# Optimization experiments

Hardware: AMD Instinct MI355X
Metric: run time of the kernel (lower is better)

Reference implementation:

```python
import jax, jax.numpy as jnp
import numpy as np

N, NTIMES, D_FEAT = 2048, 32, 128


def setup_inputs() -> dict:
    key = jax.random.key(0)
    k1, k2 = jax.random.split(key)
    return {
        "target_fairness": jnp.zeros((), dtype=jnp.float32),
        "prediction": jax.random.uniform(k1, (N, NTIMES), dtype=jnp.float32),
        "X_distance": jax.random.normal(k2, (N, D_FEAT), dtype=jnp.float32),
        "ntimes": NTIMES,
        "scale": jnp.ones((), dtype=jnp.float32),
    }


def reference(target_fairness, prediction, X_distance, ntimes, scale):
    n = prediction.shape[0]
    # cosine distance matrix: 1 - cos_sim, matches sklearn cosine_distances
    norms = jnp.linalg.norm(X_distance, axis=1, keepdims=True)
    Xn = X_distance / norms
    dist = 1.0 - Xn @ Xn.T  # [N, N]
    # pairwise |pred_j - pred_k| over all time points: [N, N, T]
    diff = jnp.abs(prediction[:, None, :] - prediction[None, :, :])
    hinge = jnp.maximum(0.0, diff - scale * dist[:, :, None])
    # only pairs k > j contribute
    mask = jnp.triu(jnp.ones((n, n), dtype=bool), k=1)
    R_beta = jnp.sum(jnp.where(mask[:, :, None], hinge, 0.0))
    model_fairness = 2.0 * R_beta / (n * (n - 1) * ntimes)
    return jnp.maximum(0.0, model_fairness - target_fairness)
```

## Files before the change

kernel.cpp:

```cpp
#include <hip/hip_runtime.h>

#define N 2048
#define T 32
#define D 128
#define BT 32
#define MT (N / BT)
#define NTILES (MT * (MT + 1) / 2)
#define NWAVES (2 * NTILES)
#define PSTR 33

typedef float floatx4 __attribute__((ext_vector_type(4)));
typedef short bf16x8 __attribute__((ext_vector_type(8)));

#define LGKM0() __builtin_amdgcn_s_waitcnt(0xc07f)

__device__ __forceinline__ void split8(float4 a, float4 b, bf16x8& h, bf16x8& l) {
  float v[8] = {a.x, a.y, a.z, a.w, b.x, b.y, b.z, b.w};
#pragma unroll
  for (int i = 0; i < 8; ++i) {
    unsigned u = __float_as_uint(v[i]);
    h[i] = (short)(u >> 16);
    float lo = v[i] - __uint_as_float(u & 0xffff0000u);
    l[i] = (short)(__float_as_uint(lo) >> 16);
  }
}

__device__ __forceinline__ float sumsq8(float4 a, float4 b) {
  return a.x * a.x + a.y * a.y + a.z * a.z + a.w * a.w +
         b.x * b.x + b.y * b.y + b.z * b.z + b.w * b.w;
}

__device__ __forceinline__ void tile_decode(int t, int& a, int& b) {
  a = (int)((2 * MT + 1 -
             sqrtf((float)((2 * MT + 1) * (2 * MT + 1) - 8 * t))) * 0.5f);
  while (a > 0 && t < a * MT - a * (a - 1) / 2) --a;
  while (t >= (a + 1) * MT - (a + 1) * a / 2) ++a;
  b = a + (t - (a * MT - a * (a - 1) / 2));
}

__global__ __launch_bounds__(64) void pair_kernel(
    const float* __restrict__ pred,
    const float* __restrict__ X,
    const float* __restrict__ scale_p,
    double* __restrict__ partials) {
  __shared__ float P[48 * PSTR];
  __shared__ float nrmA[16], nrmB[32];

  const int lane = threadIdx.x;
  const int w    = blockIdx.x;
  const int tile = w >> 1;
  const int h    = w & 1;

  int a, b;
  tile_decode(tile, a, b);
  const int aRow0 = a * BT, bRow0 = b * BT;
  const int m    = lane & 15;
  const int quad = lane >> 4;
  const float scale = scale_p[0];

#pragma unroll
  for (int s = 0; s < 6; ++s) {
    const int idx = s * 64 + lane;
    const int row = idx >> 3;
    const int fo  = (idx & 7) * 4;
    const int grow = (row < 16) ? (aRow0 + 16 * h + row) : (bRow0 + row - 16);
    *(float4*)(&P[row * PSTR + fo]) =
        *(const float4*)(pred + (size_t)grow * T + fo);
  }

  floatx4 accf[2];
  accf[0] = (floatx4){0.f, 0.f, 0.f, 0.f};
  accf[1] = (floatx4){0.f, 0.f, 0.f, 0.f};
  float ssA = 0.f, ssB[2] = {0.f, 0.f};

  const float* xar = X + (size_t)(aRow0 + 16 * h + m) * D + quad * 8;
  const float* xb0 = X + (size_t)(bRow0 + m) * D + quad * 8;

#pragma unroll
  for (int ks = 0; ks < 4; ++ks) {
    bf16x8 hA, lA, hB[2], lB[2];
    {
      float4 u0 = *(const float4*)(xar + ks * 32);
      float4 u1 = *(const float4*)(xar + ks * 32 + 4);
      ssA += sumsq8(u0, u1);
      split8(u0, u1, hA, lA);
    }
#pragma unroll
    for (int J = 0; J < 2; ++J) {
      float4 w0 = *(const float4*)(xb0 + (size_t)J * 16 * D + ks * 32);
      float4 w1 = *(const float4*)(xb0 + (size_t)J * 16 * D + ks * 32 + 4);
      ssB[J] += sumsq8(w0, w1);
      split8(w0, w1, hB[J], lB[J]);
    }
#pragma unroll
    for (int J = 0; J < 2; ++J) {
      accf[J] = __builtin_amdgcn_mfma_f32_16x16x32_bf16(hA, hB[J], accf[J], 0, 0, 0);
      accf[J] = __builtin_amdgcn_mfma_f32_16x16x32_bf16(hA, lB[J], accf[J], 0, 0, 0);
      accf[J] = __builtin_amdgcn_mfma_f32_16x16x32_bf16(lA, hB[J], accf[J], 0, 0, 0);
    }
  }

  ssA += __shfl_xor(ssA, 16, 64);
  ssA += __shfl_xor(ssA, 32, 64);
#pragma unroll
  for (int J = 0; J < 2; ++J) {
    ssB[J] += __shfl_xor(ssB[J], 16, 64);
    ssB[J] += __shfl_xor(ssB[J], 32, 64);
  }
  if (quad == 0) {
    nrmA[m]      = rsqrtf(ssA);
    nrmB[m]      = rsqrtf(ssB[0]);
    nrmB[16 + m] = rsqrtf(ssB[1]);
  }
  LGKM0();

  float na[4], nb[2];
#pragma unroll
  for (int r = 0; r < 4; ++r) na[r] = nrmA[quad * 4 + r];
  nb[0] = nrmB[m];
  nb[1] = nrmB[16 + m];

  float sd[2][4], ps[2][4];
#pragma unroll
  for (int J = 0; J < 2; ++J)
#pragma unroll
    for (int r = 0; r < 4; ++r) {
      sd[J][r] = scale * (1.0f - accf[J][r] * na[r] * nb[J]);
      ps[J][r] = 0.0f;
    }

#pragma unroll
  for (int t4 = 0; t4 < 8; ++t4) {
    float4 qb[2];
    qb[0] = *(const float4*)(&P[(16 + m) * PSTR + t4 * 4]);
    qb[1] = *(const float4*)(&P[(32 + m) * PSTR + t4 * 4]);
#pragma unroll
    for (int r = 0; r < 4; ++r) {
      float4 qa = *(const float4*)(&P[(quad * 4 + r) * PSTR + t4 * 4]);
#pragma unroll
      for (int J = 0; J < 2; ++J) {
        float s = sd[J][r];
        ps[J][r] += fmaxf(fabsf(qa.x - qb[J].x), s) +
                    fmaxf(fabsf(qa.y - qb[J].y), s) +
                    fmaxf(fabsf(qa.z - qb[J].z), s) +
                    fmaxf(fabsf(qa.w - qb[J].w), s);
      }
    }
  }

  float tsum = 0.0f;
#pragma unroll
  for (int J = 0; J < 2; ++J)
#pragma unroll
    for (int r = 0; r < 4; ++r) {
      const int ja   = aRow0 + 16 * h + quad * 4 + r;
      const int kcol = bRow0 + 16 * J + m;
      tsum += (kcol > ja) ? (ps[J][r] - 32.0f * sd[J][r]) : 0.0f;
    }

  double dsum = (double)tsum;
#pragma unroll
  for (int off = 32; off > 0; off >>= 1) dsum += __shfl_down(dsum, off, 64);
  if (lane == 0) partials[w] = dsum;
}

__global__ __launch_bounds__(256) void finalize_kernel(
    const double* __restrict__ partials, const float* __restrict__ target,
    float* __restrict__ out) {
  __shared__ double red[4];
  double s = 0.0;
  for (int i = threadIdx.x; i < NWAVES; i += 256) s += partials[i];
#pragma unroll
  for (int off = 32; off > 0; off >>= 1) s += __shfl_down(s, off, 64);
  int wave = threadIdx.x >> 6, lane = threadIdx.x & 63;
  if (lane == 0) red[wave] = s;
  __syncthreads();
  if (threadIdx.x == 0) {
    double tot = red[0] + red[1] + red[2] + red[3];
    double mf  = 2.0 * tot / ((double)N * (double)(N - 1) * (double)T);
    double r   = mf - (double)target[0];
    out[0] = (float)(r > 0.0 ? r : 0.0);
  }
}

extern "C" void kernel_launch(void* const* d_in, const int* in_sizes, int n_in,
                              void* d_out, int out_size, void* d_ws, size_t ws_size,
                              hipStream_t stream) {
  const float* target = (const float*)d_in[0];
  const float* pred   = (const float*)d_in[1];
  const float* X      = (const float*)d_in[2];
  const float* scale  = (const float*)d_in[4];

  double* partials = (double*)d_ws;

  pair_kernel<<<dim3(NWAVES), dim3(64), 0, stream>>>(pred, X, scale, partials);
  finalize_kernel<<<dim3(1), dim3(256), 0, stream>>>(partials, target,
                                                     (float*)d_out);
}
```

Before: 86.96 us.

## Pre-normalize and pre-split X into bf16 hi/lo in MFMA fragment layout

A new pre-pass kernel normalizes each row of X, splits it into bf16 high and low parts, and writes them in the exact per-lane fragment layout the MFMA loop consumes. The pair kernel then loads ready-made bf16x8 fragments instead of reloading fp32 X, recomputing norms and redoing the split for every tile, and it no longer needs the shared-memory norm exchange. This removes redundant per-tile conversion work and halves the bytes read per fragment. The cost is an extra kernel launch and workspace traffic, and normalizing before the split changes rounding slightly.

```diff
diff --git a/kernel.cpp b/kernel.cpp
--- a/kernel.cpp
+++ b/kernel.cpp
@@ -14,22 +14,6 @@
 
 #define LGKM0() __builtin_amdgcn_s_waitcnt(0xc07f)
 
-__device__ __forceinline__ void split8(float4 a, float4 b, bf16x8& h, bf16x8& l) {
-  float v[8] = {a.x, a.y, a.z, a.w, b.x, b.y, b.z, b.w};
-#pragma unroll
-  for (int i = 0; i < 8; ++i) {
-    unsigned u = __float_as_uint(v[i]);
-    h[i] = (short)(u >> 16);
-    float lo = v[i] - __uint_as_float(u & 0xffff0000u);
-    l[i] = (short)(__float_as_uint(lo) >> 16);
-  }
-}
-
-__device__ __forceinline__ float sumsq8(float4 a, float4 b) {
-  return a.x * a.x + a.y * a.y + a.z * a.z + a.w * a.w +
-         b.x * b.x + b.y * b.y + b.z * b.z + b.w * b.w;
-}
-
 __device__ __forceinline__ void tile_decode(int t, int& a, int& b) {
   a = (int)((2 * MT + 1 -
              sqrtf((float)((2 * MT + 1) * (2 * MT + 1) - 8 * t))) * 0.5f);
@@ -38,13 +22,56 @@
   b = a + (t - (a * MT - a * (a - 1) / 2));
 }
 
+__global__ __launch_bounds__(64) void presplit_kernel(
+    const float* __restrict__ X, unsigned short* __restrict__ hXt,
+    unsigned short* __restrict__ lXt) {
+  const int rb   = blockIdx.x;
+  const int lane = threadIdx.x;
+  const int m    = lane & 15;
+  const int q    = lane >> 4;
+
+  const float* xr = X + (size_t)(16 * rb + m) * D + q * 8;
+  float4 v0[4], v1[4];
+  float ss = 0.0f;
+#pragma unroll
+  for (int ks = 0; ks < 4; ++ks) {
+    v0[ks] = *(const float4*)(xr + ks * 32);
+    v1[ks] = *(const float4*)(xr + ks * 32 + 4);
+    ss += v0[ks].x * v0[ks].x + v0[ks].y * v0[ks].y +
+          v0[ks].z * v0[ks].z + v0[ks].w * v0[ks].w +
+          v1[ks].x * v1[ks].x + v1[ks].y * v1[ks].y +
+          v1[ks].z * v1[ks].z + v1[ks].w * v1[ks].w;
+  }
+  ss += __shfl_xor(ss, 16, 64);
+  ss += __shfl_xor(ss, 32, 64);
+  const float rn = rsqrtf(ss);
+
+#pragma unroll
+  for (int ks = 0; ks < 4; ++ks) {
+    bf16x8 h, l;
+    float v[8] = {v0[ks].x, v0[ks].y, v0[ks].z, v0[ks].w,
+                  v1[ks].x, v1[ks].y, v1[ks].z, v1[ks].w};
+#pragma unroll
+    for (int i = 0; i < 8; ++i) {
+      const float a = v[i] * rn;
+      const unsigned u = __float_as_uint(a);
+      h[i] = (short)(u >> 16);
+      const float lo = a - __uint_as_float(u & 0xffff0000u);
+      l[i] = (short)(__float_as_uint(lo) >> 16);
+    }
+    const size_t o = (size_t)rb * 2048 + ks * 512 + q * 128 + m * 8;
+    *(bf16x8*)(hXt + o) = h;
+    *(bf16x8*)(lXt + o) = l;
+  }
+}
+
 __global__ __launch_bounds__(64) void pair_kernel(
     const float* __restrict__ pred,
-    const float* __restrict__ X,
+    const unsigned short* __restrict__ hXt,
+    const unsigned short* __restrict__ lXt,
     const float* __restrict__ scale_p,
     double* __restrict__ partials) {
   __shared__ float P[48 * PSTR];
-  __shared__ float nrmA[16], nrmB[32];
 
   const int lane = threadIdx.x;
   const int w    = blockIdx.x;
@@ -71,26 +98,24 @@
   floatx4 accf[2];
   accf[0] = (floatx4){0.f, 0.f, 0.f, 0.f};
   accf[1] = (floatx4){0.f, 0.f, 0.f, 0.f};
-  float ssA = 0.f, ssB[2] = {0.f, 0.f};
-
-  const float* xar = X + (size_t)(aRow0 + 16 * h + m) * D + quad * 8;
-  const float* xb0 = X + (size_t)(bRow0 + m) * D + quad * 8;
+
+  const int arb = aRow0 / 16 + h;
+  const int brb = bRow0 / 16;
+  const size_t fo = (size_t)quad * 128 + m * 8;
+  const unsigned short* pa_h = hXt + (size_t)arb * 2048 + fo;
+  const unsigned short* pa_l = lXt + (size_t)arb * 2048 + fo;
+  const unsigned short* pb_h = hXt + (size_t)brb * 2048 + fo;
+  const unsigned short* pb_l = lXt + (size_t)brb * 2048 + fo;
 
 #pragma unroll
   for (int ks = 0; ks < 4; ++ks) {
     bf16x8 hA, lA, hB[2], lB[2];
-    {
-      float4 u0 = *(const float4*)(xar + ks * 32);
-      float4 u1 = *(const float4*)(xar + ks * 32 + 4);
-      ssA += sumsq8(u0, u1);
-      split8(u0, u1, hA, lA);
-    }
+    hA = *(const bf16x8*)(pa_h + ks * 512);
+    lA = *(const bf16x8*)(pa_l + ks * 512);
 #pragma unroll
     for (int J = 0; J < 2; ++J) {
-      float4 w0 = *(const float4*)(xb0 + (size_t)J * 16 * D + ks * 32);
-      float4 w1 = *(const float4*)(xb0 + (size_t)J * 16 * D + ks * 32 + 4);
-      ssB[J] += sumsq8(w0, w1);
-      split8(w0, w1, hB[J], lB[J]);
+      hB[J] = *(const bf16x8*)(pb_h + (size_t)J * 2048 + ks * 512);
+      lB[J] = *(const bf16x8*)(pb_l + (size_t)J * 2048 + ks * 512);
     }
 #pragma unroll
     for (int J = 0; J < 2; ++J) {
@@ -100,34 +125,15 @@
     }
   }
 
-  ssA += __shfl_xor(ssA, 16, 64);
-  ssA += __shfl_xor(ssA, 32, 64);
-#pragma unroll
-  for (int J = 0; J < 2; ++J) {
-    ssB[J] += __shfl_xor(ssB[J], 16, 64);
-    ssB[J] += __shfl_xor(ssB[J], 32, 64);
-  }
-  if (quad == 0) {
-    nrmA[m]      = rsqrtf(ssA);
-    nrmB[m]      = rsqrtf(ssB[0]);
-    nrmB[16 + m] = rsqrtf(ssB[1]);
-  }
+  float sd[2][4], ps[2][4];
+#pragma unroll
+  for (int J = 0; J < 2; ++J)
+#pragma unroll
+    for (int r = 0; r < 4; ++r) {
+      sd[J][r] = scale * (1.0f - accf[J][r]);
+      ps[J][r] = 0.0f;
+    }
   LGKM0();
-
-  float na[4], nb[2];
-#pragma unroll
-  for (int r = 0; r < 4; ++r) na[r] = nrmA[quad * 4 + r];
-  nb[0] = nrmB[m];
-  nb[1] = nrmB[16 + m];
-
-  float sd[2][4], ps[2][4];
-#pragma unroll
-  for (int J = 0; J < 2; ++J)
-#pragma unroll
-    for (int r = 0; r < 4; ++r) {
-      sd[J][r] = scale * (1.0f - accf[J][r] * na[r] * nb[J]);
-      ps[J][r] = 0.0f;
-    }
 
 #pragma unroll
   for (int t4 = 0; t4 < 8; ++t4) {
@@ -191,9 +197,13 @@
   const float* X      = (const float*)d_in[2];
   const float* scale  = (const float*)d_in[4];
 
-  double* partials = (double*)d_ws;
-
-  pair_kernel<<<dim3(NWAVES), dim3(64), 0, stream>>>(pred, X, scale, partials);
+  double*         partials = (double*)d_ws;
+  unsigned short* hXt = (unsigned short*)((char*)d_ws + (1u << 20));
+  unsigned short* lXt = (unsigned short*)((char*)d_ws + (2u << 20));
+
+  presplit_kernel<<<dim3(D), dim3(64), 0, stream>>>(X, hXt, lXt);
+  pair_kernel<<<dim3(NWAVES), dim3(64), 0, stream>>>(pred, hXt, lXt, scale,
+                                                     partials);
   finalize_kernel<<<dim3(1), dim3(256), 0, stream>>>(partials, target,
                                                      (float*)d_out);
 }
```

After: 80.26 us. -7.7%, faster.
